# Kernel tuning notes

Measured on AMD Instinct MI355X. Metric: run time of the kernel, lower is better.

The kernel has to match this reference:

```python
import jax, jax.numpy as jnp
import numpy as np

B, S, D = 4, 2048, 2048
H = 16
NOPE, ROPE, VD = 128, 64, 128
QK = NOPE + ROPE            # 192 per-head q/k dim
KVR = 512                   # kv_lora_rank
THETA = 10000.0
EPS = 1e-6
SCALE = QK ** -0.5


def _freqs(seq_len, d, theta):
    inv = 1.0 / (theta ** (np.arange(0, d, 2, dtype=np.float64) / d))
    ang = np.outer(np.arange(seq_len, dtype=np.float64), inv)  # [S, d//2]
    return jnp.asarray(np.cos(ang), jnp.float32), jnp.asarray(np.sin(ang), jnp.float32)


def apply_rope(x, cos, sin):
    # x: [B, S, H, d]; cos/sin: [S, d//2]; complex multiply on (even, odd) pairs
    xr = x.reshape(*x.shape[:-1], -1, 2)
    xe, xo = xr[..., 0], xr[..., 1]
    c = cos[None, :, None, :]
    s = sin[None, :, None, :]
    ye = xe * c - xo * s
    yo = xe * s + xo * c
    return jnp.stack([ye, yo], axis=-1).reshape(x.shape)


def rmsnorm(x, w, eps=EPS):
    return x * jax.lax.rsqrt(jnp.mean(x * x, axis=-1, keepdims=True) + eps) * w


def setup_inputs() -> dict:
    key = jax.random.key(0)
    ks = jax.random.split(key, 6)
    sd = 0.02
    x = jax.random.normal(ks[0], (B, S, D), jnp.float32)
    wq = jax.random.normal(ks[1], (H * QK, D), jnp.float32) * sd
    wkv_a = jax.random.normal(ks[2], (KVR + ROPE, D), jnp.float32) * sd
    kv_norm_w = jnp.ones((KVR,), jnp.float32)
    wkv_b = jax.random.normal(ks[3], (H * (NOPE + VD), KVR), jnp.float32) * sd
    wo = jax.random.normal(ks[4], (D, H * VD), jnp.float32) * sd
    cos, sin = _freqs(S, ROPE, THETA)
    return {"x": x, "wq": wq, "wkv_a": wkv_a, "kv_norm_w": kv_norm_w,
            "wkv_b": wkv_b, "wo": wo, "freqs_cos": cos, "freqs_sin": sin}


def reference(x, wq, wkv_a, kv_norm_w, wkv_b, wo, freqs_cos, freqs_sin):
    b, s, _ = x.shape
    # query projection (q_lora_rank == 0 path)
    q = jnp.einsum('bsd,ed->bse', x, wq).reshape(b, s, H, QK)
    q_nope, q_pe = q[..., :NOPE], q[..., NOPE:]
    q_pe = apply_rope(q_pe, freqs_cos, freqs_sin)

    # low-rank KV latent + decoupled rope key
    kv = jnp.einsum('bsd,ed->bse', x, wkv_a)          # [b,s,KVR+ROPE]
    kv_c, k_pe = kv[..., :KVR], kv[..., KVR:]
    k_pe = apply_rope(k_pe[:, :, None, :], freqs_cos, freqs_sin)  # [b,s,1,ROPE]
    kv_c = rmsnorm(kv_c, kv_norm_w)
    kvb = jnp.einsum('bsr,er->bse', kv_c, wkv_b).reshape(b, s, H, NOPE + VD)
    k_nope, v = kvb[..., :NOPE], kvb[..., NOPE:]
    k = jnp.concatenate([k_nope, jnp.broadcast_to(k_pe, (b, s, H, ROPE))], axis=-1)
    q_full = jnp.concatenate([q_nope, q_pe], axis=-1)

    # causal attention
    scores = jnp.einsum('bqhd,bkhd->bhqk', q_full, k) * SCALE
    mask = jnp.triu(jnp.full((s, s), -jnp.inf, jnp.float32), k=1)
    scores = scores + mask[None, None]
    p = jax.nn.softmax(scores, axis=-1)
    out = jnp.einsum('bhqk,bkhd->bqhd', p, v).reshape(b, s, H * VD)
    return jnp.einsum('bse,de->bsd', out, wo)
```

## Files before the change

### kernel.cpp

```cpp
#include <hip/hip_runtime.h>
#include <math.h>

#define BB 4
#define SS 2048
#define DD 2048
#define HH 16
#define NOPE 128
#define ROPE 64
#define VD 128
#define QKD 192
#define KVR 512
#define NP1 3712
#define ROWS (BB*SS)
#define SCL2 0.1041216338380858f

typedef __attribute__((ext_vector_type(8))) short bf16x8;
typedef __attribute__((ext_vector_type(4))) float f32x4;
typedef unsigned short bfu;
typedef __attribute__((address_space(1))) const void GV;
typedef __attribute__((address_space(3))) void LV;

__device__ __forceinline__ float bf2f(unsigned int u) {
    unsigned int i = u << 16; float f; __builtin_memcpy(&f, &i, 4); return f;
}
__device__ __forceinline__ unsigned int f2bf(float f) {
    unsigned int i; __builtin_memcpy(&i, &f, 4);
    return (i + 0x7fffu + ((i >> 16) & 1u)) >> 16;
}
__device__ __forceinline__ unsigned int cvt_pk_bf16(float lo, float hi) {
    unsigned int r;
    asm("v_cvt_pk_bf16_f32 %0, %1, %2" : "=v"(r) : "v"(lo), "v"(hi));
    return r;
}

__global__ void cast_f32_bf16(const float* __restrict__ src, bfu* __restrict__ dst,
                              long n_src, long n_dst) {
    long i = (long)blockIdx.x * blockDim.x + threadIdx.x;
    if (i * 4 >= n_dst) return;
    unsigned int lo = 0, hi = 0;
    if (i * 4 < n_src) {
        float4 v = ((const float4*)src)[i];
        lo = f2bf(v.x) | (f2bf(v.y) << 16);
        hi = f2bf(v.z) | (f2bf(v.w) << 16);
    }
    ((uint2*)dst)[i] = make_uint2(lo, hi);
}

__global__ void cast_weights(const float* __restrict__ wq, const float* __restrict__ wa,
                             const float* __restrict__ wb, const float* __restrict__ wo,
                             bfu* __restrict__ dq, bfu* __restrict__ da,
                             bfu* __restrict__ db, bfu* __restrict__ dwo) {
    long i = (long)blockIdx.x * 256 + threadIdx.x;
    const float* src; bfu* dst; long off, n_src; float scl = 1.0f;
    if (i < 1572864L)        { src = wq; dst = dq;  off = i;            n_src = 1572864L; scl = SCL2; }
    else if (i < 1900544L)   { src = wa; dst = da;  off = i - 1572864L; n_src = 294912L;  }
    else if (i < 2424832L)   { src = wb; dst = db;  off = i - 1900544L; n_src = 524288L;  }
    else if (i < 3473408L)   { src = wo; dst = dwo; off = i - 2424832L; n_src = 1048576L; }
    else return;
    unsigned int lo = 0, hi = 0;
    if (off < n_src) {
        float4 v = ((const float4*)src)[off];
        lo = f2bf(v.x * scl) | (f2bf(v.y * scl) << 16);
        hi = f2bf(v.z * scl) | (f2bf(v.w * scl) << 16);
    }
    ((uint2*)dst)[off] = make_uint2(lo, hi);
}

template <int MODE>
__global__ void __launch_bounds__(256)
gemm_bt(const bfu* __restrict__ A, const bfu* __restrict__ Bt,
        void* __restrict__ Cv, bfu* __restrict__ C2, int N, int K) {
    __shared__ __align__(16) char lds[32768];
    char* AsB = lds;
    char* BsB = lds + 16384;
    const int tid  = threadIdx.x;
    const int lane = tid & 63;
    const int wid  = tid >> 6;
    const int wr   = wid >> 1, wc = wid & 1;
    const int nwg  = gridDim.x * gridDim.y;
    const int flat = blockIdx.y * gridDim.x + blockIdx.x;
    const int swz  = (flat & 7) * (nwg >> 3) + (flat >> 3);
    const long m0 = (long)(swz / gridDim.x) * 128;
    const long n0 = (long)(swz % gridDim.x) * 128;

    f32x4 acc[4][4] = {};

    const int lr = lane >> 3;
    const int SB = (lane & 7) << 4;

    for (int k0 = 0; k0 < K; k0 += 64) {
        __syncthreads();
#pragma unroll
        for (int i = 0; i < 4; ++i) {
            int rb = wid * 32 + i * 8;
            int R  = rb + lr;
            int c  = (SB ^ ((R & 7) << 4)) >> 1;
            const bfu* gA = A  + (m0 + R) * (long)K + k0 + c;
            const bfu* gB = Bt + (n0 + R) * (long)K + k0 + c;
            __builtin_amdgcn_global_load_lds((GV*)gA, (LV*)(AsB + rb * 128), 16, 0, 0);
            __builtin_amdgcn_global_load_lds((GV*)gB, (LV*)(BsB + rb * 128), 16, 0, 0);
        }
        __syncthreads();
#pragma unroll
        for (int kk = 0; kk < 2; ++kk) {
            bf16x8 av[4], bv[4];
            const int cb = kk * 64 + ((lane >> 4) << 4);
#pragma unroll
            for (int m = 0; m < 4; ++m) {
                int R = wr * 64 + m * 16 + (lane & 15);
                av[m] = *(const bf16x8*)(AsB + R * 128 + (cb ^ ((R & 7) << 4)));
            }
#pragma unroll
            for (int n = 0; n < 4; ++n) {
                int R = wc * 64 + n * 16 + (lane & 15);
                bv[n] = *(const bf16x8*)(BsB + R * 128 + (cb ^ ((R & 7) << 4)));
            }
#pragma unroll
            for (int m = 0; m < 4; ++m)
#pragma unroll
                for (int n = 0; n < 4; ++n)
                    acc[m][n] = __builtin_amdgcn_mfma_f32_16x16x32_bf16(av[m], bv[n], acc[m][n], 0, 0, 0);
        }
    }

    const int cr = (lane >> 4) << 2;
    const int cc = lane & 15;
#pragma unroll
    for (int m = 0; m < 4; ++m)
#pragma unroll
        for (int n = 0; n < 4; ++n)
#pragma unroll
            for (int r = 0; r < 4; ++r) {
                long row = m0 + wr * 64 + m * 16 + cr + r;
                long col = n0 + wc * 64 + n * 16 + cc;
                float val = acc[m][n][r];
                if (MODE == 1) {
                    ((float*)Cv)[row * N + col] = val;
                } else if (MODE == 2) {
                    long b_ = row >> 11;
                    long s  = row & 2047;
                    long h  = col >> 8;
                    long wi = col & 255;
                    if (wi < 128)
                        C2[((b_ * HH + h) * SS + s) * (long)QKD + wi] = (bfu)f2bf(val);
                    else
                        ((bfu*)Cv)[row * 2048 + h * 128 + (wi - 128)] = (bfu)f2bf(val);
                } else {
                    long b_ = row >> 11;
                    long s  = row & 2047;
                    if (col < 3072) {
                        unsigned int h = (unsigned int)col / 192u;
                        unsigned int d = (unsigned int)col - h * 192u;
                        ((bfu*)Cv)[((b_ * HH + h) * SS + s) * (long)QKD + d] = (bfu)f2bf(val);
                    } else {
                        C2[row * 640 + (col - 3072)] = (bfu)f2bf(val);
                    }
                }
            }
}

__global__ void rope_pe_fill(bfu* __restrict__ qr, const bfu* __restrict__ kpe,
                             bfu* __restrict__ kall,
                             const float* __restrict__ fc, const float* __restrict__ fs) {
    long t = (long)blockIdx.x * 256 + threadIdx.x;
    int  ch = (int)(t & 7);
    long r  = t >> 3;
    int  s  = (int)(r & 2047);
    long bh = (r >> 11) & 63;
    long b_ = bh >> 4;
    if (t < 1048576L) {
        bfu* p = qr + (bh * SS + s) * (long)QKD + NOPE + ch * 8;
        bf16x8 v = *(const bf16x8*)p;
        int i0 = ch * 4;
        unsigned int out[4];
#pragma unroll
        for (int k = 0; k < 4; ++k) {
            float e = bf2f((unsigned short)v[2 * k]);
            float o = bf2f((unsigned short)v[2 * k + 1]);
            float c = fc[s * 32 + i0 + k], sn = fs[s * 32 + i0 + k];
            out[k] = cvt_pk_bf16(e * c - o * sn, e * sn + o * c);
        }
        *(uint4*)p = make_uint4(out[0], out[1], out[2], out[3]);
    } else {
        bf16x8 v = *(const bf16x8*)(kpe + (b_ * SS + s) * (long)ROPE + ch * 8);
        *(bf16x8*)(kall + (bh * SS + s) * (long)QKD + NOPE + ch * 8) = v;
    }
}

__global__ void __launch_bounds__(256)
rms_rope_kv(const bfu* __restrict__ kv1, const float* __restrict__ wn,
            bfu* __restrict__ kvc, bfu* __restrict__ kpe,
            const float* __restrict__ fc, const float* __restrict__ fs) {
    const int row = blockIdx.x;
    const int t   = threadIdx.x;
    const int s   = row & (SS - 1);
    const long base = (long)row * 640;
    unsigned int v = *(const unsigned int*)(kv1 + base + 2 * t);
    float a = bf2f(v & 0xffff), c2 = bf2f(v >> 16);
    float ssum = a * a + c2 * c2;
#pragma unroll
    for (int d = 1; d < 64; d <<= 1) ssum += __shfl_xor(ssum, d);
    __shared__ float red[4];
    const int lane = t & 63, w = t >> 6;
    if (lane == 0) red[w] = ssum;
    __syncthreads();
    float tot = red[0] + red[1] + red[2] + red[3];
    float scale = rsqrtf(tot * (1.0f / 512.0f) + 1e-6f);
    float w0 = wn[2 * t], w1 = wn[2 * t + 1];
    unsigned int out = f2bf(a * scale * w0) | (f2bf(c2 * scale * w1) << 16);
    *(unsigned int*)(kvc + (long)row * KVR + 2 * t) = out;
    if (t < 32) {
        unsigned int pv = *(const unsigned int*)(kv1 + base + KVR + 2 * t);
        float e = bf2f(pv & 0xffff), o = bf2f(pv >> 16);
        float cc = fc[s * 32 + t], sn = fs[s * 32 + t];
        unsigned int po = f2bf(e * cc - o * sn) | (f2bf(e * sn + o * cc) << 16);
        *(unsigned int*)(kpe + (long)row * ROPE + 2 * t) = po;
    }
}

__global__ void __launch_bounds__(256)
transpose_v2(const bfu* __restrict__ vpack, bfu* __restrict__ vt) {
    __shared__ __align__(16) char tile[64 * 256];
    const int tid = threadIdx.x;
    const int bid = blockIdx.x;
    const int st  = bid & 31;
    const int bh  = bid >> 5;
    const int h   = bh & 15;
    const long b_ = bh >> 4;
    const long sbase = b_ * SS + st * 64;
#pragma unroll
    for (int i = 0; i < 4; ++i) {
        int idx = i * 256 + tid;
        int row = idx >> 4;
        int ch  = (idx & 15) ^ ((row >> 3) & 7);
        const bfu* src = vpack + (sbase + row) * 2048 + h * 128 + ch * 8;
        __builtin_amdgcn_global_load_lds((GV*)src, (LV*)(tile + idx * 16), 16, 0, 0);
    }
    __syncthreads();
#pragma unroll
    for (int i = 0; i < 4; ++i) {
        int idx = i * 256 + tid;
        int sc = idx & 7;
        int v  = (idx >> 3) & 127;
        bfu tmp[8];
#pragma unroll
        for (int k = 0; k < 8; ++k) {
            int row = sc * 8 + k;
            tmp[k] = *(const bfu*)(tile + row * 256 + (((v >> 3) ^ ((row >> 3) & 7)) << 4) + (v & 7) * 2);
        }
        *(bf16x8*)(vt + ((long)bh * VD + v) * SS + st * 64 + sc * 8) = *(bf16x8*)tmp;
    }
}

template <bool MASKED>
__device__ __forceinline__ void attn_tile64(
    const char* kbuf, const char* vbuf, char* pw,
    const bf16x8 (&qf)[6], f32x4 (&accv)[8],
    float& ms, float& ls, int kv0, int qa, int ql, int kg, int lane) {
    f32x4 sc[4] = {};
#pragma unroll
    for (int j = 0; j < 4; ++j)
#pragma unroll
        for (int d = 0; d < 6; ++d) {
            int row  = j * 16 + ql;
            int slot = (d * 4 + kg) ^ (ql & 7);
            bf16x8 kf = *(const bf16x8*)(kbuf + row * 384 + slot * 16);
            sc[j] = __builtin_amdgcn_mfma_f32_16x16x32_bf16(kf, qf[d], sc[j], 0, 0, 0);
        }
    float p[4][4];
    float mx = -1e30f;
#pragma unroll
    for (int j = 0; j < 4; ++j)
#pragma unroll
        for (int r = 0; r < 4; ++r) {
            float s = sc[j][r];
            if (MASKED) {
                int kv = kv0 + j * 16 + kg * 4 + r;
                s = (kv > qa) ? -1e30f : s;
            }
            p[j][r] = s;
            mx = fmaxf(mx, s);
        }
    mx = fmaxf(mx, __shfl_xor(mx, 16));
    mx = fmaxf(mx, __shfl_xor(mx, 32));
    float rs = 0.f;
    if (__all(mx <= ms)) {
#pragma unroll
        for (int j = 0; j < 4; ++j)
#pragma unroll
            for (int r = 0; r < 4; ++r) {
                float e = exp2f(p[j][r] - ms);
                p[j][r] = e;
                rs += e;
            }
        rs += __shfl_xor(rs, 16);
        rs += __shfl_xor(rs, 32);
        ls += rs;
    } else {
        float mn = fmaxf(ms, mx);
        float al = exp2f(ms - mn);
        ms = mn;
#pragma unroll
        for (int j = 0; j < 4; ++j)
#pragma unroll
            for (int r = 0; r < 4; ++r) {
                float e = exp2f(p[j][r] - mn);
                p[j][r] = e;
                rs += e;
            }
        rs += __shfl_xor(rs, 16);
        rs += __shfl_xor(rs, 32);
        ls = ls * al + rs;
        float alT[4];
#pragma unroll
        for (int r = 0; r < 4; ++r)
            alT[r] = __shfl(al, (lane & 48) + kg * 4 + r);
#pragma unroll
        for (int v8 = 0; v8 < 8; ++v8)
#pragma unroll
            for (int r = 0; r < 4; ++r)
                accv[v8][r] *= alT[r];
    }
#pragma unroll
    for (int j = 0; j < 4; ++j) {
        uint2 u;
        u.x = cvt_pk_bf16(p[j][0], p[j][1]);
        u.y = cvt_pk_bf16(p[j][2], p[j][3]);
        int slot = (2 * j + (kg >> 1)) ^ (ql & 7);
        *(uint2*)(pw + ql * 128 + slot * 16 + (kg & 1) * 8) = u;
    }
    asm volatile("s_waitcnt lgkmcnt(0)" ::: "memory");
#pragma unroll
    for (int t2 = 0; t2 < 2; ++t2) {
        int ps = (t2 * 4 + kg) ^ (ql & 7);
        bf16x8 pa = *(const bf16x8*)(pw + ql * 128 + ps * 16);
#pragma unroll
        for (int v8 = 0; v8 < 8; ++v8) {
            int vrow = v8 * 16 + ql;
            int vs   = (t2 * 4 + kg) ^ (ql & 7);
            bf16x8 vf = *(const bf16x8*)(vbuf + vrow * 128 + vs * 16);
            accv[v8] = __builtin_amdgcn_mfma_f32_16x16x32_bf16(pa, vf, accv[v8], 0, 0, 0);
        }
    }
}

__global__ void __launch_bounds__(512)
attn(const bfu* __restrict__ qr, const bfu* __restrict__ kall,
     const bfu* __restrict__ vt, bfu* __restrict__ ao) {
    __shared__ __align__(16) char kbuf[2][64 * 384];
    __shared__ __align__(16) char vbuf[2][128 * 128];
    __shared__ __align__(16) char pbuf[8][2048];
    const int tid  = threadIdx.x;
    const int lane = tid & 63;
    const int w    = tid >> 6;
    const int ql   = lane & 15;
    const int kg   = lane >> 4;
    const int bid  = blockIdx.x;
    const int qb   = 15 - (bid >> 6);
    const int bh   = bid & 63;
    const int h    = bh & 15;
    const int b    = bh >> 4;
    const char* Q  = (const char*)(qr + (long)bh * SS * QKD);
    const char* Kp = (const char*)(kall + (long)bh * SS * QKD);
    const char* Vp = (const char*)(vt + (long)bh * VD * SS);
    char* pw = pbuf[w];

    const int qa_min = qb * 128 + w * 16;
    const int qa = qa_min + ql;

    const char* ksrc[3]; int kdst[3];
#pragma unroll
    for (int i = 0; i < 3; ++i) {
        int idx  = i * 512 + tid;
        int row  = idx / 24;
        int slot = idx - row * 24;
        int ss   = slot ^ (row & 7);
        ksrc[i]  = Kp + (long)row * 384 + ss * 16;
        kdst[i]  = idx * 16;
    }
    const char* vsrc[2]; int vdst[2];
#pragma unroll
    for (int i = 0; i < 2; ++i) {
        int idx  = i * 512 + tid;
        int row  = idx >> 3;
        int slot = idx & 7;
        int ss   = slot ^ (row & 7);
        vsrc[i]  = Vp + (long)row * (SS * 2) + ss * 16;
        vdst[i]  = idx * 16;
    }
    auto stage = [&](int bi, int kv0) {
        const long ko = (long)kv0 * 384;
        const long vo = (long)kv0 * 2;
#pragma unroll
        for (int i = 0; i < 3; ++i)
            __builtin_amdgcn_global_load_lds((GV*)(ksrc[i] + ko), (LV*)(kbuf[bi] + kdst[i]), 16, 0, 0);
#pragma unroll
        for (int i = 0; i < 2; ++i)
            __builtin_amdgcn_global_load_lds((GV*)(vsrc[i] + vo), (LV*)(vbuf[bi] + vdst[i]), 16, 0, 0);
    };

    bf16x8 qf[6];
#pragma unroll
    for (int d = 0; d < 6; ++d)
        qf[d] = *(const bf16x8*)(Q + (long)(qa_min + ql) * 384 + d * 64 + kg * 16);

    f32x4 accv[8] = {};
    float ms = -1e30f, ls = 0.f;
    const int ntiles = 2 * qb + 2;

    stage(0, 0);
    __syncthreads();

    for (int t = 0; t < ntiles; ++t) {
        const int cur = t & 1;
        const int kv0 = t * 64;
        if (t + 1 < ntiles)
            stage(cur ^ 1, kv0 + 64);
        if (kv0 + 63 <= qa_min)
            attn_tile64<false>(kbuf[cur], vbuf[cur], pw, qf, accv, ms, ls, kv0, qa, ql, kg, lane);
        else if (kv0 <= qa_min + 15)
            attn_tile64<true>(kbuf[cur], vbuf[cur], pw, qf, accv, ms, ls, kv0, qa, ql, kg, lane);
        asm volatile("s_waitcnt vmcnt(0)" ::: "memory");
        __builtin_amdgcn_s_barrier();
        asm volatile("" ::: "memory");
    }
    float li[4];
#pragma unroll
    for (int r = 0; r < 4; ++r)
        li[r] = 1.0f / __shfl(ls, (lane & 48) + kg * 4 + r);
#pragma unroll
    for (int v8 = 0; v8 < 8; ++v8)
#pragma unroll
        for (int r = 0; r < 4; ++r) {
            float o = accv[v8][r] * li[r];
            long row = (long)b * SS + qa_min + kg * 4 + r;
            ao[row * (long)(HH * VD) + h * VD + v8 * 16 + ql] = (bfu)f2bf(o);
        }
}

#define O_XB   0L
#define O_WQ   33554432L
#define O_WA   46137344L
#define O_WB   48758784L
#define O_WO   52953088L
#define O_KALL 61341696L
#define O_KV1  111673344L
#define O_QR   122159104L
#define O_KVC  172490752L
#define O_KPE  180879360L
#define O_AO   181927936L
#define WS_NEED 215482368L

extern "C" void kernel_launch(void* const* d_in, const int* in_sizes, int n_in,
                              void* d_out, int out_size, void* d_ws, size_t ws_size,
                              hipStream_t stream) {
    const float* x      = (const float*)d_in[0];
    const float* wq     = (const float*)d_in[1];
    const float* wkv_a  = (const float*)d_in[2];
    const float* kvnw   = (const float*)d_in[3];
    const float* wkv_b  = (const float*)d_in[4];
    const float* wo     = (const float*)d_in[5];
    const float* fcos   = (const float*)d_in[6];
    const float* fsin   = (const float*)d_in[7];
    if (ws_size < (size_t)WS_NEED) return;

    char* ws = (char*)d_ws;
    bfu* xb   = (bfu*)(ws + O_XB);
    bfu* wqb  = (bfu*)(ws + O_WQ);
    bfu* wab  = (bfu*)(ws + O_WA);
    bfu* wbb  = (bfu*)(ws + O_WB);
    bfu* wob  = (bfu*)(ws + O_WO);
    bfu* kall = (bfu*)(ws + O_KALL);
    bfu* kv1  = (bfu*)(ws + O_KV1);
    bfu* qr   = (bfu*)(ws + O_QR);
    bfu* kvc  = (bfu*)(ws + O_KVC);
    bfu* kpe  = (bfu*)(ws + O_KPE);
    bfu* ao   = (bfu*)(ws + O_AO);
    bfu* vt   = xb;
    bfu* vpack = (bfu*)d_out;

    cast_f32_bf16<<<16384, 256, 0, stream>>>(x, xb, 16777216L, 16777216L);
    cast_weights<<<13568, 256, 0, stream>>>(wq, wkv_a, wkv_b, wo, wqb, wab, wbb, wob);

    gemm_bt<3><<<dim3(29, 64), 256, 0, stream>>>(xb, wqb, qr, kv1, NP1, DD);

    rms_rope_kv<<<ROWS, 256, 0, stream>>>(kv1, kvnw, kvc, kpe, fcos, fsin);

    gemm_bt<2><<<dim3(32, 64), 256, 0, stream>>>(kvc, wbb, vpack, kall, HH * 256, KVR);

    rope_pe_fill<<<8192, 256, 0, stream>>>(qr, kpe, kall, fcos, fsin);
    transpose_v2<<<2048, 256, 0, stream>>>(vpack, vt);

    attn<<<1024, 512, 0, stream>>>(qr, kall, vt, ao);

    gemm_bt<1><<<dim3(16, 64), 256, 0, stream>>>(ao, wob, d_out, nullptr, DD, HH * VD);
}
```

Measured before the change: 508.2 us.

## Split kv_b GEMM into K and transposed-V GEMMs, merge casts, prioritize MFMA

Merges the x cast and the weight casts into a single kernel that also splits wkv_b into separate K and V weight matrices. The V projection is now a swapped-operand GEMM that writes V directly in the transposed [b,h,v,s] layout, so the separate transpose kernel and the intermediate vpack buffer are no longer needed. s_setprio is also raised around the MFMA sections of the attention tile. The trade-off is an extra GEMM launch and strided epilogue stores along the sequence dimension.

```diff
diff --git a/kernel.cpp b/kernel.cpp
--- a/kernel.cpp
+++ b/kernel.cpp
@@ -33,29 +33,30 @@
     return r;
 }
 
-__global__ void cast_f32_bf16(const float* __restrict__ src, bfu* __restrict__ dst,
-                              long n_src, long n_dst) {
-    long i = (long)blockIdx.x * blockDim.x + threadIdx.x;
-    if (i * 4 >= n_dst) return;
-    unsigned int lo = 0, hi = 0;
-    if (i * 4 < n_src) {
-        float4 v = ((const float4*)src)[i];
-        lo = f2bf(v.x) | (f2bf(v.y) << 16);
-        hi = f2bf(v.z) | (f2bf(v.w) << 16);
-    }
-    ((uint2*)dst)[i] = make_uint2(lo, hi);
-}
-
-__global__ void cast_weights(const float* __restrict__ wq, const float* __restrict__ wa,
-                             const float* __restrict__ wb, const float* __restrict__ wo,
-                             bfu* __restrict__ dq, bfu* __restrict__ da,
-                             bfu* __restrict__ db, bfu* __restrict__ dwo) {
+__global__ void cast_all(const float* __restrict__ x, const float* __restrict__ wq,
+                         const float* __restrict__ wa, const float* __restrict__ wb,
+                         const float* __restrict__ wo,
+                         bfu* __restrict__ dx, bfu* __restrict__ dq,
+                         bfu* __restrict__ da, bfu* __restrict__ dkb,
+                         bfu* __restrict__ dvb, bfu* __restrict__ dwo) {
     long i = (long)blockIdx.x * 256 + threadIdx.x;
     const float* src; bfu* dst; long off, n_src; float scl = 1.0f;
-    if (i < 1572864L)        { src = wq; dst = dq;  off = i;            n_src = 1572864L; scl = SCL2; }
-    else if (i < 1900544L)   { src = wa; dst = da;  off = i - 1572864L; n_src = 294912L;  }
-    else if (i < 2424832L)   { src = wb; dst = db;  off = i - 1900544L; n_src = 524288L;  }
-    else if (i < 3473408L)   { src = wo; dst = dwo; off = i - 2424832L; n_src = 1048576L; }
+    if (i < 4194304L)        { src = x;  dst = dx;  off = i;            n_src = 4194304L; }
+    else if (i < 5767168L)   { src = wq; dst = dq;  off = i - 4194304L; n_src = 1572864L; scl = SCL2; }
+    else if (i < 6094848L)   { src = wa; dst = da;  off = i - 5767168L; n_src = 294912L;  }
+    else if (i < 6619136L)   {
+        long off2 = i - 6094848L;
+        long row = off2 >> 7, c = off2 & 127;
+        long h = row >> 8, wi = row & 255;
+        bfu* d2 = (wi < 128) ? dkb : dvb;
+        long drow = (h << 7) + (wi & 127);
+        float4 v = ((const float4*)wb)[off2];
+        unsigned int lo = f2bf(v.x) | (f2bf(v.y) << 16);
+        unsigned int hi = f2bf(v.z) | (f2bf(v.w) << 16);
+        ((uint2*)d2)[drow * 128 + c] = make_uint2(lo, hi);
+        return;
+    }
+    else if (i < 7667712L)   { src = wo; dst = dwo; off = i - 6619136L; n_src = 1048576L; }
     else return;
     unsigned int lo = 0, hi = 0;
     if (off < n_src) {
@@ -139,13 +140,10 @@
                 } else if (MODE == 2) {
                     long b_ = row >> 11;
                     long s  = row & 2047;
-                    long h  = col >> 8;
-                    long wi = col & 255;
-                    if (wi < 128)
-                        C2[((b_ * HH + h) * SS + s) * (long)QKD + wi] = (bfu)f2bf(val);
-                    else
-                        ((bfu*)Cv)[row * 2048 + h * 128 + (wi - 128)] = (bfu)f2bf(val);
-                } else {
+                    long h  = col >> 7;
+                    long d  = col & 127;
+                    C2[((b_ * HH + h) * SS + s) * (long)QKD + d] = (bfu)f2bf(val);
+                } else if (MODE == 3) {
                     long b_ = row >> 11;
                     long s  = row & 2047;
                     if (col < 3072) {
@@ -155,6 +153,12 @@
                     } else {
                         C2[row * 640 + (col - 3072)] = (bfu)f2bf(val);
                     }
+                } else {
+                    long h  = row >> 7;
+                    long v  = row & 127;
+                    long b_ = col >> 11;
+                    long s  = col & 2047;
+                    ((bfu*)Cv)[(((b_ * HH + h) * VD) + v) * SS + s] = (bfu)f2bf(val);
                 }
             }
 }
@@ -218,46 +222,13 @@
     }
 }
 
-__global__ void __launch_bounds__(256)
-transpose_v2(const bfu* __restrict__ vpack, bfu* __restrict__ vt) {
-    __shared__ __align__(16) char tile[64 * 256];
-    const int tid = threadIdx.x;
-    const int bid = blockIdx.x;
-    const int st  = bid & 31;
-    const int bh  = bid >> 5;
-    const int h   = bh & 15;
-    const long b_ = bh >> 4;
-    const long sbase = b_ * SS + st * 64;
-#pragma unroll
-    for (int i = 0; i < 4; ++i) {
-        int idx = i * 256 + tid;
-        int row = idx >> 4;
-        int ch  = (idx & 15) ^ ((row >> 3) & 7);
-        const bfu* src = vpack + (sbase + row) * 2048 + h * 128 + ch * 8;
-        __builtin_amdgcn_global_load_lds((GV*)src, (LV*)(tile + idx * 16), 16, 0, 0);
-    }
-    __syncthreads();
-#pragma unroll
-    for (int i = 0; i < 4; ++i) {
-        int idx = i * 256 + tid;
-        int sc = idx & 7;
-        int v  = (idx >> 3) & 127;
-        bfu tmp[8];
-#pragma unroll
-        for (int k = 0; k < 8; ++k) {
-            int row = sc * 8 + k;
-            tmp[k] = *(const bfu*)(tile + row * 256 + (((v >> 3) ^ ((row >> 3) & 7)) << 4) + (v & 7) * 2);
-        }
-        *(bf16x8*)(vt + ((long)bh * VD + v) * SS + st * 64 + sc * 8) = *(bf16x8*)tmp;
-    }
-}
-
 template <bool MASKED>
 __device__ __forceinline__ void attn_tile64(
     const char* kbuf, const char* vbuf, char* pw,
     const bf16x8 (&qf)[6], f32x4 (&accv)[8],
     float& ms, float& ls, int kv0, int qa, int ql, int kg, int lane) {
     f32x4 sc[4] = {};
+    __builtin_amdgcn_s_setprio(1);
 #pragma unroll
     for (int j = 0; j < 4; ++j)
 #pragma unroll
@@ -267,6 +238,7 @@
             bf16x8 kf = *(const bf16x8*)(kbuf + row * 384 + slot * 16);
             sc[j] = __builtin_amdgcn_mfma_f32_16x16x32_bf16(kf, qf[d], sc[j], 0, 0, 0);
         }
+    __builtin_amdgcn_s_setprio(0);
     float p[4][4];
     float mx = -1e30f;
 #pragma unroll
@@ -330,6 +302,7 @@
         *(uint2*)(pw + ql * 128 + slot * 16 + (kg & 1) * 8) = u;
     }
     asm volatile("s_waitcnt lgkmcnt(0)" ::: "memory");
+    __builtin_amdgcn_s_setprio(1);
 #pragma unroll
     for (int t2 = 0; t2 < 2; ++t2) {
         int ps = (t2 * 4 + kg) ^ (ql & 7);
@@ -342,6 +315,7 @@
             accv[v8] = __builtin_amdgcn_mfma_f32_16x16x32_bf16(pa, vf, accv[v8], 0, 0, 0);
         }
     }
+    __builtin_amdgcn_s_setprio(0);
 }
 
 __global__ void __launch_bounds__(512)
@@ -441,7 +415,8 @@
 #define O_XB   0L
 #define O_WQ   33554432L
 #define O_WA   46137344L
-#define O_WB   48758784L
+#define O_WKB  48758784L
+#define O_WVB  50855936L
 #define O_WO   52953088L
 #define O_KALL 61341696L
 #define O_KV1  111673344L
@@ -468,7 +443,8 @@
     bfu* xb   = (bfu*)(ws + O_XB);
     bfu* wqb  = (bfu*)(ws + O_WQ);
     bfu* wab  = (bfu*)(ws + O_WA);
-    bfu* wbb  = (bfu*)(ws + O_WB);
+    bfu* wkb  = (bfu*)(ws + O_WKB);
+    bfu* wvb  = (bfu*)(ws + O_WVB);
     bfu* wob  = (bfu*)(ws + O_WO);
     bfu* kall = (bfu*)(ws + O_KALL);
     bfu* kv1  = (bfu*)(ws + O_KV1);
@@ -477,19 +453,20 @@
     bfu* kpe  = (bfu*)(ws + O_KPE);
     bfu* ao   = (bfu*)(ws + O_AO);
     bfu* vt   = xb;
-    bfu* vpack = (bfu*)d_out;
-
-    cast_f32_bf16<<<16384, 256, 0, stream>>>(x, xb, 16777216L, 16777216L);
-    cast_weights<<<13568, 256, 0, stream>>>(wq, wkv_a, wkv_b, wo, wqb, wab, wbb, wob);
+    (void)wab;
+
+    cast_all<<<29952, 256, 0, stream>>>(x, wq, wkv_a, wkv_b, wo,
+                                        xb, wqb, wab, wkb, wvb, wob);
 
     gemm_bt<3><<<dim3(29, 64), 256, 0, stream>>>(xb, wqb, qr, kv1, NP1, DD);
 
     rms_rope_kv<<<ROWS, 256, 0, stream>>>(kv1, kvnw, kvc, kpe, fcos, fsin);
 
-    gemm_bt<2><<<dim3(32, 64), 256, 0, stream>>>(kvc, wbb, vpack, kall, HH * 256, KVR);
+    gemm_bt<2><<<dim3(16, 64), 256, 0, stream>>>(kvc, wkb, nullptr, kall, 2048, KVR);
+
+    gemm_bt<4><<<dim3(64, 16), 256, 0, stream>>>(wvb, kvc, vt, nullptr, 8192, KVR);
 
     rope_pe_fill<<<8192, 256, 0, stream>>>(qr, kpe, kall, fcos, fsin);
-    transpose_v2<<<2048, 256, 0, stream>>>(vpack, vt);
 
     attn<<<1024, 512, 0, stream>>>(qr, kall, vt, ao);
 
```

Measured after the change: 513.2 us. No clear change (+1.0%).
